# Optimization experiments

Hardware: AMD Instinct MI355X
Metric: run time of the kernel (lower is better)

The kernel has to match this reference:

```python
import jax, jax.numpy as jnp
import numpy as np

B, L, D_MODEL, COND = 2, 2048, 1024, 1024
D_STATE, EXPAND = 64, 2
D_INNER = EXPAND * D_MODEL
MLP_H = 2 * D_MODEL  # mlp_expansion=2
EPS = 1e-5


def setup_inputs() -> dict:
    key = jax.random.key(0)
    ks = jax.random.split(key, 24)
    p = lambda i, shape, s=0.02: (jax.random.normal(ks[i], shape, jnp.float32) * s)
    inp = {
        "x": jax.random.normal(ks[0], (B, L, D_MODEL), jnp.float32),
        "c": jax.random.normal(ks[1], (B, COND), jnp.float32),
        "adaln_mamba_w": p(2, (COND, 3 * D_MODEL)),
        "adaln_mamba_b": jnp.zeros((3 * D_MODEL,), jnp.float32),
        "adaln_mlp_w": p(3, (COND, 3 * D_MODEL)),
        "adaln_mlp_b": jnp.zeros((3 * D_MODEL,), jnp.float32),
        "mlp_w1": p(4, (D_MODEL, MLP_H)),
        "mlp_w2": p(5, (D_MODEL, MLP_H)),
        "mlp_w3": p(6, (MLP_H, D_MODEL)),
    }
    a_init = jnp.log(jnp.tile(jnp.arange(1, D_STATE + 1, dtype=jnp.float32), (D_INNER, 1)))
    for j, pre in enumerate(["fwd", "bwd"]):
        o = 7 + 6 * j
        inp[f"{pre}_in_w"] = p(o, (D_MODEL, 2 * D_INNER))
        inp[f"{pre}_xproj_w"] = p(o + 1, (D_INNER, D_INNER + 2 * D_STATE))
        inp[f"{pre}_dt_bias"] = jnp.zeros((D_INNER,), jnp.float32)
        inp[f"{pre}_A_log"] = a_init
        inp[f"{pre}_D"] = jnp.ones((D_INNER,), jnp.float32)
        inp[f"{pre}_out_w"] = p(o + 2, (D_INNER, D_MODEL))
    return inp


def _adaln(x, c, w, b):
    mod = (c @ w + b)[:, None, :]  # (B,1,3D)
    shift, scale, gate = jnp.split(mod, 3, axis=-1)
    mu = jnp.mean(x, axis=-1, keepdims=True)
    var = jnp.var(x, axis=-1, keepdims=True)
    normed = (x - mu) * jax.lax.rsqrt(var + EPS) * (1.0 + scale) + shift
    return normed, gate


def _ssm(h, in_w, xproj_w, dt_bias, A_log, Dskip, out_w):
    """Selective-SSM: h (B,L,D) -> (B,L,D)."""
    xz = h @ in_w                      # (B,L,2*di)
    xs, z = jnp.split(xz, 2, axis=-1)
    xs = jax.nn.silu(xs)               # (B,L,di)
    proj = xs @ xproj_w                # (B,L,di+2*ds)
    dt = jax.nn.softplus(proj[..., :D_INNER] + dt_bias)        # (B,L,di)
    Bm = proj[..., D_INNER:D_INNER + D_STATE]                  # (B,L,ds)
    Cm = proj[..., D_INNER + D_STATE:]                         # (B,L,ds)
    A = -jnp.exp(A_log)                                        # (di,ds)

    def step(hst, ins):
        dt_t, B_t, C_t, x_t = ins  # (B,di),(B,ds),(B,ds),(B,di)
        dA = jnp.exp(dt_t[:, :, None] * A)                     # (B,di,ds)
        hst = hst * dA + (dt_t * x_t)[:, :, None] * B_t[:, None, :]
        y_t = jnp.einsum('bds,bs->bd', hst, C_t)
        return hst, y_t

    tm = lambda a: jnp.swapaxes(a, 0, 1)  # time-major
    h0 = jnp.zeros((h.shape[0], D_INNER, D_STATE), h.dtype)
    _, ys = jax.lax.scan(step, h0, (tm(dt), tm(Bm), tm(Cm), tm(xs)))
    y = jnp.swapaxes(ys, 0, 1) + xs * Dskip
    return (y * jax.nn.silu(z)) @ out_w


def reference(x, c, adaln_mamba_w, adaln_mamba_b, adaln_mlp_w, adaln_mlp_b,
              mlp_w1, mlp_w2, mlp_w3,
              fwd_in_w, fwd_xproj_w, fwd_dt_bias, fwd_A_log, fwd_D, fwd_out_w,
              bwd_in_w, bwd_xproj_w, bwd_dt_bias, bwd_A_log, bwd_D, bwd_out_w):
    h, gate = _adaln(x, c, adaln_mamba_w, adaln_mamba_b)
    h_fwd = _ssm(h, fwd_in_w, fwd_xproj_w, fwd_dt_bias, fwd_A_log, fwd_D, fwd_out_w)
    h_bwd = jnp.flip(_ssm(jnp.flip(h, 1), bwd_in_w, bwd_xproj_w, bwd_dt_bias, bwd_A_log, bwd_D, bwd_out_w), 1)
    x = x + gate * (h_fwd + h_bwd)
    h, gate = _adaln(x, c, adaln_mlp_w, adaln_mlp_b)
    mlp_out = (jax.nn.silu(h @ mlp_w1) * (h @ mlp_w2)) @ mlp_w3
    return x + gate * mlp_out
```

## Files before the change

kernel.cpp:

```cpp
#include <hip/hip_runtime.h>
#include <hip/hip_bf16.h>
#include <math.h>

#define B_SZ 2
#define LSEQ 2048
#define DM   1024
#define DI   2048
#define NTOK (B_SZ*LSEQ)
#define EPSV 1e-5f

typedef __attribute__((ext_vector_type(8))) short short8v;
typedef __attribute__((ext_vector_type(4))) short short4v;
typedef __attribute__((ext_vector_type(4))) float f4v;

static __device__ __forceinline__ float sigmoidf_(float v) {
    return 1.f / (1.f + __expf(-v));
}
static __device__ __forceinline__ float softplus_(float v) {
    return fmaxf(v, 0.f) + log1pf(__expf(-fabsf(v)));
}
static __device__ __forceinline__ short f2bf(float f) {
    __hip_bfloat16 h = __float2bfloat16(f);
    return *reinterpret_cast<short*>(&h);
}

__global__ __launch_bounds__(256) void mod_kernel(const float* __restrict__ c,
                                                  const float* __restrict__ w,
                                                  const float* __restrict__ bias,
                                                  float* __restrict__ mod) {
    int jt = blockIdx.x * 32;
    int jj = threadIdx.x & 31, ks = threadIdx.x >> 5;
    int j = jt + jj;
    const float* c0 = c;
    const float* c1 = c + 1024;
    float a0 = 0.f, a1 = 0.f;
    int k0 = ks * 128;
#pragma unroll 4
    for (int k = k0; k < k0 + 128; ++k) {
        float wv = w[(size_t)k * 3072 + j];
        a0 = fmaf(c0[k], wv, a0);
        a1 = fmaf(c1[k], wv, a1);
    }
    __shared__ float red[2][8][32];
    red[0][ks][jj] = a0;
    red[1][ks][jj] = a1;
    __syncthreads();
    if (threadIdx.x < 64) {
        int bb = threadIdx.x >> 5, j2 = threadIdx.x & 31;
        float s = bias[jt + j2];
#pragma unroll
        for (int kk = 0; kk < 8; ++kk) s += red[bb][kk][j2];
        mod[bb * 3072 + jt + j2] = s;
    }
}

__global__ __launch_bounds__(256) void adaln_kernel(const float* __restrict__ x,
                                                    const float* __restrict__ mod,
                                                    __hip_bfloat16* __restrict__ h) {
    int row = blockIdx.x;
    int b = row >> 11;
    const float* xr = x + (size_t)row * DM;
    float v[4], s = 0.f, s2 = 0.f;
#pragma unroll
    for (int i = 0; i < 4; ++i) {
        v[i] = xr[threadIdx.x + i * 256];
        s += v[i]; s2 += v[i] * v[i];
    }
#pragma unroll
    for (int off = 32; off; off >>= 1) { s += __shfl_xor(s, off); s2 += __shfl_xor(s2, off); }
    __shared__ float red[8];
    int wid = threadIdx.x >> 6;
    if ((threadIdx.x & 63) == 0) { red[wid] = s; red[4 + wid] = s2; }
    __syncthreads();
    s  = red[0] + red[1] + red[2] + red[3];
    s2 = red[4] + red[5] + red[6] + red[7];
    float mu  = s * (1.f / DM);
    float var = s2 * (1.f / DM) - mu * mu;
    float rstd = rsqrtf(var + EPSV);
    const float* mb = mod + b * 3072;
    __hip_bfloat16* hr = h + (size_t)row * DM;
#pragma unroll
    for (int i = 0; i < 4; ++i) {
        int d = threadIdx.x + i * 256;
        hr[d] = __float2bfloat16((v[i] - mu) * rstd * (1.f + mb[1024 + d]) + mb[d]);
    }
}

template <int ACCUM>
__global__ __launch_bounds__(256) void gemm_bf16_kernel(
    const short* __restrict__ A, int lda,
    const short* __restrict__ Bt, int ldb,
    float* __restrict__ C, int ldc, int K)
{
    __shared__ short As[128][40];
    __shared__ short Bs[128][40];
    int tid = threadIdx.x;
    int m0 = blockIdx.y * 128, n0 = blockIdx.x * 128;
    int wave = tid >> 6, lane = tid & 63;
    int wm = (wave & 1) * 64, wn = (wave >> 1) * 64;
    int srow = tid >> 2, sq = (tid & 3) * 8;
    const short* aptr = A + (size_t)(m0 + srow) * lda + sq;
    const short* bptr = Bt + (size_t)(n0 + srow) * ldb + sq;
    int fr = lane & 15, fq = lane >> 4;
    f4v acc[4][4];
#pragma unroll
    for (int i = 0; i < 4; ++i)
#pragma unroll
        for (int j = 0; j < 4; ++j) acc[i][j] = (f4v){0.f, 0.f, 0.f, 0.f};

    short8v a0 = *(const short8v*)(aptr);
    short8v a1 = *(const short8v*)(aptr + 64 * (size_t)lda);
    short8v b0 = *(const short8v*)(bptr);
    short8v b1 = *(const short8v*)(bptr + 64 * (size_t)ldb);
    for (int k0 = 0; k0 < K; k0 += 32) {
        __syncthreads();
        *(short8v*)&As[srow][sq]      = a0;
        *(short8v*)&As[srow + 64][sq] = a1;
        *(short8v*)&Bs[srow][sq]      = b0;
        *(short8v*)&Bs[srow + 64][sq] = b1;
        __syncthreads();
        if (k0 + 32 < K) {
            a0 = *(const short8v*)(aptr + k0 + 32);
            a1 = *(const short8v*)(aptr + 64 * (size_t)lda + k0 + 32);
            b0 = *(const short8v*)(bptr + k0 + 32);
            b1 = *(const short8v*)(bptr + 64 * (size_t)ldb + k0 + 32);
        }
        short8v af[4], bf[4];
#pragma unroll
        for (int i = 0; i < 4; ++i) af[i] = *(const short8v*)&As[wm + i * 16 + fr][fq * 8];
#pragma unroll
        for (int j = 0; j < 4; ++j) bf[j] = *(const short8v*)&Bs[wn + j * 16 + fr][fq * 8];
#pragma unroll
        for (int i = 0; i < 4; ++i)
#pragma unroll
            for (int j = 0; j < 4; ++j)
                acc[i][j] = __builtin_amdgcn_mfma_f32_16x16x32_bf16(af[i], bf[j], acc[i][j], 0, 0, 0);
    }
#pragma unroll
    for (int i = 0; i < 4; ++i)
#pragma unroll
        for (int j = 0; j < 4; ++j) {
#pragma unroll
            for (int r = 0; r < 4; ++r) {
                int row = m0 + wm + i * 16 + fq * 4 + r;
                int col = n0 + wn + j * 16 + fr;
                float* cp = C + (size_t)row * ldc + col;
                if (ACCUM) *cp += acc[i][j][r]; else *cp = acc[i][j][r];
            }
        }
}

__global__ __launch_bounds__(256) void wcast_kernel(const float* __restrict__ w,
                                                    int K, int N,
                                                    short* __restrict__ wT) {
    __shared__ short tile[32][33];
    int c0 = blockIdx.x * 32, r0 = blockIdx.y * 32;
    int tx = threadIdx.x & 31, ty = threadIdx.x >> 5;
#pragma unroll
    for (int i = 0; i < 32; i += 8)
        tile[ty + i][tx] = f2bf(w[(size_t)(r0 + ty + i) * N + c0 + tx]);
    __syncthreads();
#pragma unroll
    for (int i = 0; i < 32; i += 8)
        wT[(size_t)(c0 + ty + i) * K + r0 + tx] = tile[tx][ty + i];
}

__global__ void silu_xs_kernel(float* __restrict__ xz, __hip_bfloat16* __restrict__ xsb) {
    int idx = blockIdx.x * 256 + threadIdx.x;
    int row = idx >> 9, c = (idx & 511) << 2;
    float4* p = (float4*)(xz + (size_t)row * 4096 + c);
    float4 v = *p;
    v.x *= sigmoidf_(v.x); v.y *= sigmoidf_(v.y);
    v.z *= sigmoidf_(v.z); v.w *= sigmoidf_(v.w);
    *p = v;
    short4v s = {f2bf(v.x), f2bf(v.y), f2bf(v.z), f2bf(v.w)};
    *(short4v*)((short*)xsb + (size_t)row * 2048 + c) = s;
}

__global__ __launch_bounds__(256) void transpose_inplace_kernel(float* __restrict__ M) {
    int bj = blockIdx.x, bi = blockIdx.y;
    if (bi > bj) return;
    __shared__ float ta[32][33], tb[32][33];
    int tx = threadIdx.x & 31, ty = threadIdx.x >> 5;
    size_t oA = ((size_t)bi * 32) * 4096 + (size_t)bj * 32;
    size_t oB = ((size_t)bj * 32) * 4096 + (size_t)bi * 32;
#pragma unroll
    for (int i = 0; i < 32; i += 8)
        ta[ty + i][tx] = M[oA + (size_t)(ty + i) * 4096 + tx];
    if (bi != bj) {
#pragma unroll
        for (int i = 0; i < 32; i += 8)
            tb[ty + i][tx] = M[oB + (size_t)(ty + i) * 4096 + tx];
    }
    __syncthreads();
#pragma unroll
    for (int i = 0; i < 32; i += 8)
        M[oB + (size_t)(ty + i) * 4096 + tx] = ta[tx][ty + i];
    if (bi != bj) {
#pragma unroll
        for (int i = 0; i < 32; i += 8)
            M[oA + (size_t)(ty + i) * 4096 + tx] = tb[tx][ty + i];
    }
}

__global__ __launch_bounds__(256) void transpose_dt_kernel(const float* __restrict__ proj,
                                                           const float* __restrict__ bias,
                                                           short* __restrict__ dtT) {
    __shared__ short tile[32][33];
    int c0 = blockIdx.x * 32, r0 = blockIdx.y * 32;
    int tx = threadIdx.x & 31, ty = threadIdx.x >> 5;
#pragma unroll
    for (int i = 0; i < 32; i += 8) {
        float v = proj[(size_t)(r0 + ty + i) * 2176 + c0 + tx];
        tile[ty + i][tx] = f2bf(softplus_(v + bias[c0 + tx]));
    }
    __syncthreads();
#pragma unroll
    for (int i = 0; i < 32; i += 8)
        dtT[(size_t)(c0 + ty + i) * 4096 + r0 + tx] = tile[tx][ty + i];
}

__global__ __launch_bounds__(256) void transpose_bf16_kernel(const short* __restrict__ in,
                                                             short* __restrict__ outp) {
    __shared__ short tile[32][33];
    int c0 = blockIdx.x * 32, r0 = blockIdx.y * 32;
    int tx = threadIdx.x & 31, ty = threadIdx.x >> 5;
#pragma unroll
    for (int i = 0; i < 32; i += 8)
        tile[ty + i][tx] = in[(size_t)(r0 + ty + i) * 4096 + c0 + tx];
    __syncthreads();
#pragma unroll
    for (int i = 0; i < 32; i += 8)
        outp[(size_t)(c0 + ty + i) * 2048 + r0 + tx] = tile[tx][ty + i];
}

#define SLOAD(ib, s0_)                                                   \
    _Pragma("unroll")                                                    \
    for (int i_ = 0; i_ < 8; ++i_) {                                     \
        int sl_ = (s0_) + i_;  sl_ = sl_ > (LSEQ-1) ? (LSEQ-1) : sl_;    \
        int tm_ = REV ? (LSEQ-1) - sl_ : sl_;                            \
        dts[ib][i_]  = __bfloat162float(sdt[tm_]);                       \
        xss[ib][i_]  = sxs[tm_];                                         \
        Bbuf[ib][i_] = projB[(size_t)tm_ * 2176 + lane];                 \
        Cbuf[ib][i_] = projB[(size_t)tm_ * 2176 + 64 + lane];            \
    }

#define SCOMP(ib, r0_)                                                   \
    _Pragma("unroll")                                                    \
    for (int i_ = 0; i_ < 8; ++i_) {                                     \
        float e_ = __builtin_amdgcn_exp2f(dts[ib][i_] * Ae);             \
        float u_ = dts[ib][i_] * xss[ib][i_];                            \
        hst = fmaf(hst, e_, u_ * Bbuf[ib][i_]);                          \
        Lw[((r0_) + i_) * 65] = hst * Cbuf[ib][i_];                      \
    }

template <int REV>
__global__ __launch_bounds__(256) void scan_kernel(
    const float* __restrict__ proj,
    const __hip_bfloat16* __restrict__ dtT,
    const float* __restrict__ xzT,
    const float* __restrict__ A_log, const float* __restrict__ Dsk,
    __hip_bfloat16* __restrict__ yT)
{
    __shared__ float lds[4][32 * 65];
    int lane = threadIdx.x & 63;
    int wv4 = threadIdx.x >> 6;
    int wave = blockIdx.x * 4 + wv4;
    int b = __builtin_amdgcn_readfirstlane(wave >> 11);
    int d = __builtin_amdgcn_readfirstlane(wave & 2047);
    float A  = -__expf(A_log[d * 64 + lane]);
    float Ae = A * 1.44269504f;
    float Dv = Dsk[d];
    const float* projB = proj + (size_t)b * LSEQ * 2176 + 2048;
    const __hip_bfloat16* sdt = dtT + (size_t)d * 4096 + b * 2048;
    const float* sxs = xzT + (size_t)d * 4096 + b * 2048;
    const float* szz = xzT + (size_t)(2048 + d) * 4096 + b * 2048;
    __hip_bfloat16* yrow = yT + (size_t)d * 4096 + b * 2048;
    float* Lw = &lds[wv4][0] + lane;
    const float* Lr = &lds[wv4][0] + (lane & 31) * 65 + (lane >> 5) * 32;
    float hst = 0.f;

    float dts[2][8], xss[2][8], Bbuf[2][8], Cbuf[2][8];
    SLOAD(0, 0);
    for (int s0 = 0; s0 < LSEQ; s0 += 32) {
        SLOAD(1, s0 + 8);  SCOMP(0, 0);
        SLOAD(0, s0 + 16); SCOMP(1, 8);
        SLOAD(1, s0 + 24); SCOMP(0, 16);
        SLOAD(0, s0 + 32); SCOMP(1, 24);
        float ssum = 0.f;
#pragma unroll
        for (int k = 0; k < 32; ++k) ssum += Lr[k];
        ssum += __shfl_xor(ssum, 32);
        if (lane < 32) {
            int tm = REV ? (LSEQ - 1) - (s0 + lane) : (s0 + lane);
            float xv = sxs[tm];
            float zv = szz[tm];
            yrow[tm] = __float2bfloat16(fmaf(xv, Dv, ssum) * (zv * sigmoidf_(zv)));
        }
    }
}

__global__ void gated_add_kernel(const float* __restrict__ x, const float* __restrict__ v,
                                 const float* __restrict__ mod, float* __restrict__ out) {
    int idx = blockIdx.x * 256 + threadIdx.x;
    int row = idx >> 8, b = row >> 11, c = (idx & 255) << 2;
    size_t o = (size_t)row * 1024 + c;
    float4 xv = *(const float4*)(x + o);
    float4 hv = *(const float4*)(v + o);
    float4 gv = *(const float4*)(mod + b * 3072 + 2048 + c);
    float4 r = {fmaf(gv.x, hv.x, xv.x), fmaf(gv.y, hv.y, xv.y),
                fmaf(gv.z, hv.z, xv.z), fmaf(gv.w, hv.w, xv.w)};
    *(float4*)(out + o) = r;
}

__global__ void silumul_kernel(const float* __restrict__ a, const float* __restrict__ bb,
                               __hip_bfloat16* __restrict__ g) {
    int idx = blockIdx.x * 256 + threadIdx.x;
    size_t o = (size_t)idx << 2;
    float4 av = *(const float4*)(a + o);
    float4 bv = *(const float4*)(bb + o);
    short4v r = {f2bf(av.x * sigmoidf_(av.x) * bv.x), f2bf(av.y * sigmoidf_(av.y) * bv.y),
                 f2bf(av.z * sigmoidf_(av.z) * bv.z), f2bf(av.w * sigmoidf_(av.w) * bv.w)};
    *(short4v*)((short*)g + o) = r;
}

extern "C" void kernel_launch(void* const* d_in, const int* in_sizes, int n_in,
                              void* d_out, int out_size, void* d_ws, size_t ws_size,
                              hipStream_t stream) {
    const float* x         = (const float*)d_in[0];
    const float* c         = (const float*)d_in[1];
    const float* adw_mamba = (const float*)d_in[2];
    const float* adb_mamba = (const float*)d_in[3];
    const float* adw_mlp   = (const float*)d_in[4];
    const float* adb_mlp   = (const float*)d_in[5];
    const float* mlp_w1    = (const float*)d_in[6];
    const float* mlp_w2    = (const float*)d_in[7];
    const float* mlp_w3    = (const float*)d_in[8];
    const float* in_w[2]    = {(const float*)d_in[9],  (const float*)d_in[15]};
    const float* xproj_w[2] = {(const float*)d_in[10], (const float*)d_in[16]};
    const float* dt_bias[2] = {(const float*)d_in[11], (const float*)d_in[17]};
    const float* A_log[2]   = {(const float*)d_in[12], (const float*)d_in[18]};
    const float* Dsk[2]     = {(const float*)d_in[13], (const float*)d_in[19]};
    const float* out_w[2]   = {(const float*)d_in[14], (const float*)d_in[20]};
    float* out = (float*)d_out;

    float* ws    = (float*)d_ws;
    float* mod   = ws;
    short* h_bf  = (short*)(ws + 12288);
    float* xz    = ws + 12288 + 2097152;
    float* proj  = xz + 16777216;
    float* scr   = proj + 8912896;
    short* xs_bf = (short*)scr;
    short* dtT   = (short*)scr;
    short* ybtok = (short*)scr;
    short* yTb   = (short*)(scr + 4194304);
    float* hsum  = scr + 8388608;
    short* wb    = (short*)(hsum + 4194304);
    short* inw_b[2]  = {wb,            wb + 4194304};
    short* xpj_b[2]  = {wb + 8388608,  wb + 12845056};
    short* outw_b[2] = {wb + 17301504, wb + 19398656};
    short* w1_b = wb + 21495808;
    short* w2_b = wb + 23592960;
    short* w3_b = wb + 25690112;

    dim3 blk(256);

    for (int dir = 0; dir < 2; ++dir) {
        wcast_kernel<<<dim3(128, 32), blk, 0, stream>>>(in_w[dir],   1024, 4096, inw_b[dir]);
        wcast_kernel<<<dim3(68, 64),  blk, 0, stream>>>(xproj_w[dir],2048, 2176, xpj_b[dir]);
        wcast_kernel<<<dim3(32, 64),  blk, 0, stream>>>(out_w[dir],  2048, 1024, outw_b[dir]);
    }
    wcast_kernel<<<dim3(64, 32), blk, 0, stream>>>(mlp_w1, 1024, 2048, w1_b);
    wcast_kernel<<<dim3(64, 32), blk, 0, stream>>>(mlp_w2, 1024, 2048, w2_b);
    wcast_kernel<<<dim3(32, 64), blk, 0, stream>>>(mlp_w3, 2048, 1024, w3_b);

    mod_kernel<<<96, blk, 0, stream>>>(c, adw_mamba, adb_mamba, mod);
    mod_kernel<<<96, blk, 0, stream>>>(c, adw_mlp,   adb_mlp,   mod + 6144);
    adaln_kernel<<<NTOK, blk, 0, stream>>>(x, mod, (__hip_bfloat16*)h_bf);

    for (int dir = 0; dir < 2; ++dir) {
        gemm_bf16_kernel<0><<<dim3(32, 32), blk, 0, stream>>>(h_bf, 1024, inw_b[dir], 1024, xz, 4096, 1024);
        silu_xs_kernel<<<8192, blk, 0, stream>>>(xz, (__hip_bfloat16*)xs_bf);
        gemm_bf16_kernel<0><<<dim3(17, 32), blk, 0, stream>>>(xs_bf, 2048, xpj_b[dir], 2048, proj, 2176, 2048);
        transpose_inplace_kernel<<<dim3(128, 128), blk, 0, stream>>>(xz);
        transpose_dt_kernel<<<dim3(64, 128), blk, 0, stream>>>(proj, dt_bias[dir], dtT);
        if (dir == 0)
            scan_kernel<0><<<1024, blk, 0, stream>>>(proj, (const __hip_bfloat16*)dtT, xz,
                                                     A_log[dir], Dsk[dir], (__hip_bfloat16*)yTb);
        else
            scan_kernel<1><<<1024, blk, 0, stream>>>(proj, (const __hip_bfloat16*)dtT, xz,
                                                     A_log[dir], Dsk[dir], (__hip_bfloat16*)yTb);
        transpose_bf16_kernel<<<dim3(128, 64), blk, 0, stream>>>(yTb, ybtok);
        if (dir == 0)
            gemm_bf16_kernel<0><<<dim3(8, 32), blk, 0, stream>>>(ybtok, 2048, outw_b[dir], 2048, hsum, 1024, 2048);
        else
            gemm_bf16_kernel<1><<<dim3(8, 32), blk, 0, stream>>>(ybtok, 2048, outw_b[dir], 2048, hsum, 1024, 2048);
    }

    gated_add_kernel<<<4096, blk, 0, stream>>>(x, hsum, mod, out);
    adaln_kernel<<<NTOK, blk, 0, stream>>>(out, mod + 6144, (__hip_bfloat16*)h_bf);
    gemm_bf16_kernel<0><<<dim3(16, 32), blk, 0, stream>>>(h_bf, 1024, w1_b, 1024, xz, 2048, 1024);
    gemm_bf16_kernel<0><<<dim3(16, 32), blk, 0, stream>>>(h_bf, 1024, w2_b, 1024, xz + (size_t)NTOK * 2048, 2048, 1024);
    silumul_kernel<<<8192, blk, 0, stream>>>(xz, xz + (size_t)NTOK * 2048, (__hip_bfloat16*)yTb);
    gemm_bf16_kernel<0><<<dim3(8, 32), blk, 0, stream>>>(yTb, 2048, w3_b, 2048, hsum, 1024, 2048);
    gated_add_kernel<<<4096, blk, 0, stream>>>(out, hsum, mod + 6144, out);
}
```

Measured before the change: 1.258 ms.

## Use direct global-to-LDS loads in GEMM and pack B/C for scan

The bf16 GEMM now stages its tiles with global_load_lds 16-byte transfers straight into unpadded LDS. This replaces the register-prefetch plus ds_write path but drops the software prefetch overlap and the padding that avoided bank conflicts. A new bcpack kernel interleaves the B and C projection columns into a compact 128-float-per-row buffer, so each scan step reads one float2 instead of two strided loads from the wide proj matrix. The clamp on the scan load index was also removed, which assumes the prefetch never runs past the sequence end.

```diff
diff --git a/kernel.cpp b/kernel.cpp
--- a/kernel.cpp
+++ b/kernel.cpp
@@ -23,6 +23,11 @@
     __hip_bfloat16 h = __float2bfloat16(f);
     return *reinterpret_cast<short*>(&h);
 }
+
+#define GLDS16(g, l)                                                        \
+    __builtin_amdgcn_global_load_lds(                                       \
+        (const __attribute__((address_space(1))) void*)(g),                 \
+        (__attribute__((address_space(3))) void*)(l), 16, 0, 0)
 
 __global__ __launch_bounds__(256) void mod_kernel(const float* __restrict__ c,
                                                   const float* __restrict__ w,
@@ -92,15 +97,22 @@
     const short* __restrict__ Bt, int ldb,
     float* __restrict__ C, int ldc, int K)
 {
-    __shared__ short As[128][40];
-    __shared__ short Bs[128][40];
+    __shared__ short As[128 * 32];
+    __shared__ short Bs[128 * 32];
     int tid = threadIdx.x;
     int m0 = blockIdx.y * 128, n0 = blockIdx.x * 128;
     int wave = tid >> 6, lane = tid & 63;
     int wm = (wave & 1) * 64, wn = (wave >> 1) * 64;
-    int srow = tid >> 2, sq = (tid & 3) * 8;
-    const short* aptr = A + (size_t)(m0 + srow) * lda + sq;
-    const short* bptr = Bt + (size_t)(n0 + srow) * ldb + sq;
+    int srow = wave * 16 + (lane >> 2);
+    int scol = (lane & 3) * 8;
+    const short* aptr0 = A  + (size_t)(m0 + srow) * lda + scol;
+    const short* aptr1 = aptr0 + (size_t)64 * lda;
+    const short* bptr0 = Bt + (size_t)(n0 + srow) * ldb + scol;
+    const short* bptr1 = bptr0 + (size_t)64 * ldb;
+    short* lA0 = As + wave * 512;
+    short* lA1 = As + 2048 + wave * 512;
+    short* lB0 = Bs + wave * 512;
+    short* lB1 = Bs + 2048 + wave * 512;
     int fr = lane & 15, fq = lane >> 4;
     f4v acc[4][4];
 #pragma unroll
@@ -108,28 +120,18 @@
 #pragma unroll
         for (int j = 0; j < 4; ++j) acc[i][j] = (f4v){0.f, 0.f, 0.f, 0.f};
 
-    short8v a0 = *(const short8v*)(aptr);
-    short8v a1 = *(const short8v*)(aptr + 64 * (size_t)lda);
-    short8v b0 = *(const short8v*)(bptr);
-    short8v b1 = *(const short8v*)(bptr + 64 * (size_t)ldb);
     for (int k0 = 0; k0 < K; k0 += 32) {
         __syncthreads();
-        *(short8v*)&As[srow][sq]      = a0;
-        *(short8v*)&As[srow + 64][sq] = a1;
-        *(short8v*)&Bs[srow][sq]      = b0;
-        *(short8v*)&Bs[srow + 64][sq] = b1;
+        GLDS16(aptr0 + k0, lA0);
+        GLDS16(aptr1 + k0, lA1);
+        GLDS16(bptr0 + k0, lB0);
+        GLDS16(bptr1 + k0, lB1);
         __syncthreads();
-        if (k0 + 32 < K) {
-            a0 = *(const short8v*)(aptr + k0 + 32);
-            a1 = *(const short8v*)(aptr + 64 * (size_t)lda + k0 + 32);
-            b0 = *(const short8v*)(bptr + k0 + 32);
-            b1 = *(const short8v*)(bptr + 64 * (size_t)ldb + k0 + 32);
-        }
         short8v af[4], bf[4];
 #pragma unroll
-        for (int i = 0; i < 4; ++i) af[i] = *(const short8v*)&As[wm + i * 16 + fr][fq * 8];
-#pragma unroll
-        for (int j = 0; j < 4; ++j) bf[j] = *(const short8v*)&Bs[wn + j * 16 + fr][fq * 8];
+        for (int i = 0; i < 4; ++i) af[i] = *(const short8v*)&As[(wm + i * 16 + fr) * 32 + fq * 8];
+#pragma unroll
+        for (int j = 0; j < 4; ++j) bf[j] = *(const short8v*)&Bs[(wn + j * 16 + fr) * 32 + fq * 8];
 #pragma unroll
         for (int i = 0; i < 4; ++i)
 #pragma unroll
@@ -220,6 +222,14 @@
         dtT[(size_t)(c0 + ty + i) * 4096 + r0 + tx] = tile[tx][ty + i];
 }
 
+__global__ void bcpack_kernel(const float* __restrict__ proj, float* __restrict__ bcp) {
+    int idx = blockIdx.x * 256 + threadIdx.x;
+    int row = idx >> 7, j = idx & 127;
+    float v = proj[(size_t)row * 2176 + 2048 + j];
+    int s = j & 63, half = j >> 6;
+    bcp[(size_t)row * 128 + s * 2 + half] = v;
+}
+
 __global__ __launch_bounds__(256) void transpose_bf16_kernel(const short* __restrict__ in,
                                                              short* __restrict__ outp) {
     __shared__ short tile[32][33];
@@ -237,12 +247,12 @@
 #define SLOAD(ib, s0_)                                                   \
     _Pragma("unroll")                                                    \
     for (int i_ = 0; i_ < 8; ++i_) {                                     \
-        int sl_ = (s0_) + i_;  sl_ = sl_ > (LSEQ-1) ? (LSEQ-1) : sl_;    \
-        int tm_ = REV ? (LSEQ-1) - sl_ : sl_;                            \
-        dts[ib][i_]  = __bfloat162float(sdt[tm_]);                       \
-        xss[ib][i_]  = sxs[tm_];                                         \
-        Bbuf[ib][i_] = projB[(size_t)tm_ * 2176 + lane];                 \
-        Cbuf[ib][i_] = projB[(size_t)tm_ * 2176 + 64 + lane];            \
+        int tm_ = REV ? (LSEQ - 1) - ((s0_) + i_) : ((s0_) + i_);        \
+        dts[ib][i_] = __bfloat162float(sdt[tm_]);                        \
+        xss[ib][i_] = sxs[tm_];                                          \
+        float2 bcv_ = sbc[(size_t)tm_ * 64 + lane];                      \
+        Bbuf[ib][i_] = bcv_.x;                                           \
+        Cbuf[ib][i_] = bcv_.y;                                           \
     }
 
 #define SCOMP(ib, r0_)                                                   \
@@ -256,7 +266,7 @@
 
 template <int REV>
 __global__ __launch_bounds__(256) void scan_kernel(
-    const float* __restrict__ proj,
+    const float* __restrict__ bcp,
     const __hip_bfloat16* __restrict__ dtT,
     const float* __restrict__ xzT,
     const float* __restrict__ A_log, const float* __restrict__ Dsk,
@@ -271,7 +281,7 @@
     float A  = -__expf(A_log[d * 64 + lane]);
     float Ae = A * 1.44269504f;
     float Dv = Dsk[d];
-    const float* projB = proj + (size_t)b * LSEQ * 2176 + 2048;
+    const float2* sbc = (const float2*)bcp + (size_t)b * LSEQ * 64;
     const __hip_bfloat16* sdt = dtT + (size_t)d * 4096 + b * 2048;
     const float* sxs = xzT + (size_t)d * 4096 + b * 2048;
     const float* szz = xzT + (size_t)(2048 + d) * 4096 + b * 2048;
@@ -355,7 +365,8 @@
     short* ybtok = (short*)scr;
     short* yTb   = (short*)(scr + 4194304);
     float* hsum  = scr + 8388608;
-    short* wb    = (short*)(hsum + 4194304);
+    float* bcp   = hsum + 4194304 + 4096;
+    short* wb    = (short*)(bcp + 524288 + 4096);
     short* inw_b[2]  = {wb,            wb + 4194304};
     short* xpj_b[2]  = {wb + 8388608,  wb + 12845056};
     short* outw_b[2] = {wb + 17301504, wb + 19398656};
@@ -384,11 +395,12 @@
         gemm_bf16_kernel<0><<<dim3(17, 32), blk, 0, stream>>>(xs_bf, 2048, xpj_b[dir], 2048, proj, 2176, 2048);
         transpose_inplace_kernel<<<dim3(128, 128), blk, 0, stream>>>(xz);
         transpose_dt_kernel<<<dim3(64, 128), blk, 0, stream>>>(proj, dt_bias[dir], dtT);
+        bcpack_kernel<<<2048, blk, 0, stream>>>(proj, bcp);
         if (dir == 0)
-            scan_kernel<0><<<1024, blk, 0, stream>>>(proj, (const __hip_bfloat16*)dtT, xz,
+            scan_kernel<0><<<1024, blk, 0, stream>>>(bcp, (const __hip_bfloat16*)dtT, xz,
                                                      A_log[dir], Dsk[dir], (__hip_bfloat16*)yTb);
         else
-            scan_kernel<1><<<1024, blk, 0, stream>>>(proj, (const __hip_bfloat16*)dtT, xz,
+            scan_kernel<1><<<1024, blk, 0, stream>>>(bcp, (const __hip_bfloat16*)dtT, xz,
                                                      A_log[dir], Dsk[dir], (__hip_bfloat16*)yTb);
         transpose_bf16_kernel<<<dim3(128, 64), blk, 0, stream>>>(yTb, ybtok);
         if (dir == 0)
```

New measurement: 1.487 ms. 18.2% more time.
